# Optimization experiments

Hardware: AMD Instinct MI355X
Metric: run time of the kernel (lower is better)

Reference implementation:

```python
import jax, jax.numpy as jnp
import numpy as np

B, T, C = 2, 2048, 1024
NH = 16
HS = C // NH


def setup_inputs() -> dict:
    key = jax.random.key(0)
    k1, k2, k3 = jax.random.split(key, 3)
    scale = 1.0 / np.sqrt(C)
    return {
        "x": jax.random.normal(k1, (B, T, C), dtype=jnp.float32),
        "W_attn": jax.random.normal(k2, (C, 3 * C), dtype=jnp.float32) * scale,
        "b_attn": jnp.zeros((3 * C,), dtype=jnp.float32),
        "W_proj": jax.random.normal(k3, (C, C), dtype=jnp.float32) * scale,
        "b_proj": jnp.zeros((C,), dtype=jnp.float32),
    }


def reference(x, W_attn, b_attn, W_proj, b_proj) -> jnp.ndarray:
    Bx, Tx, Cx = x.shape
    qkv = x @ W_attn + b_attn                      # [B, T, 3C]
    q, k, v = jnp.split(qkv, 3, axis=-1)           # each [B, T, C]

    def heads(t):  # [B, T, C] -> [B, NH, T, HS]
        return t.reshape(Bx, Tx, NH, HS).transpose(0, 2, 1, 3)

    q, k, v = heads(q), heads(k), heads(v)
    att = jnp.einsum("bhqd,bhkd->bhqk", q, k) / jnp.sqrt(jnp.float32(HS))
    causal = jnp.tril(jnp.ones((Tx, Tx), dtype=bool))
    att = jnp.where(causal, att, -jnp.inf)
    att = jax.nn.softmax(att, axis=-1)
    y = jnp.einsum("bhqk,bhkd->bhqd", att, v)      # [B, NH, T, HS]
    y = y.transpose(0, 2, 1, 3).reshape(Bx, Tx, Cx)
    return y @ W_proj + b_proj
```

## Files before the change

### kernel.cpp

```cpp
#include <hip/hip_runtime.h>
#include <hip/hip_bf16.h>
#include <stdint.h>

#define DEV static __device__ __forceinline__

typedef __attribute__((ext_vector_type(8))) __bf16 bf16x8;
typedef __attribute__((ext_vector_type(4))) __bf16 bf16x4;
typedef __attribute__((ext_vector_type(4))) float f32x4;
typedef __attribute__((ext_vector_type(16))) float f32x16;

#define BB 2
#define TT 2048
#define CC 1024
#define NHH 16
#define HSS 64
#define BT 4096
#define N3 3072

DEV unsigned short f2bf(float f) {
  union { float f; uint32_t u; } v; v.f = f;
  uint32_t r = v.u + 0x7FFFu + ((v.u >> 16) & 1u);
  return (unsigned short)(r >> 16);
}

typedef const __attribute__((address_space(1))) unsigned int* gas_t;
typedef __attribute__((address_space(3))) unsigned int* las_t;

DEV void glds16(const void* g, void* l) {
  __builtin_amdgcn_global_load_lds((gas_t)g, (las_t)l, 16, 0, 0);
}

DEV f32x4 mfma16(bf16x8 a, bf16x8 b, f32x4 c) {
  return __builtin_amdgcn_mfma_f32_16x16x32_bf16(a, b, c, 0, 0, 0);
}
DEV f32x16 mfma32(bf16x8 a, bf16x8 b, f32x16 c) {
  return __builtin_amdgcn_mfma_f32_32x32x16_bf16(a, b, c, 0, 0, 0);
}

DEV bf16x8 ld8(const unsigned short* p) { return *(const bf16x8*)p; }

DEV f32x16 z16() {
  f32x16 v;
#pragma unroll
  for (int i = 0; i < 16; i++) v[i] = 0.f;
  return v;
}

__global__ void k_conv(const float* __restrict__ in, unsigned short* __restrict__ out, int n4) {
  int i = blockIdx.x * blockDim.x + threadIdx.x;
  int stride = gridDim.x * blockDim.x;
  for (; i < n4; i += stride) {
    float4 v = ((const float4*)in)[i];
    ushort4 o;
    o.x = f2bf(v.x); o.y = f2bf(v.y); o.z = f2bf(v.z); o.w = f2bf(v.w);
    ((ushort4*)out)[i] = o;
  }
}

__global__ void k_transp(const float* __restrict__ in, unsigned short* __restrict__ out,
                         int K, int N) {
  __shared__ float tile[32][33];
  int n0 = blockIdx.x * 32, k0 = blockIdx.y * 32;
  int tx = threadIdx.x, ty = threadIdx.y;
  for (int r = ty; r < 32; r += 8)
    tile[r][tx] = in[(size_t)(k0 + r) * N + n0 + tx];
  __syncthreads();
  for (int r = ty; r < 32; r += 8)
    out[(size_t)(n0 + r) * K + k0 + tx] = f2bf(tile[tx][r]);
}

template <int OUT_BF16>
__global__ __launch_bounds__(256) void k_gemm(const unsigned short* __restrict__ A,
                                              const unsigned short* __restrict__ Bt,
                                              const float* __restrict__ bias,
                                              void* __restrict__ Cout,
                                              int M, int N, int K) {
  __shared__ __align__(16) unsigned short As[128 * 32];
  __shared__ __align__(16) unsigned short Bs[128 * 32];
  const int t = threadIdx.x;
  const int wave = t >> 6, l = t & 63, lr = l & 15, lg = l >> 4;
  const int m0 = blockIdx.y * 128, n0 = blockIdx.x * 128;
  const int wm = wave >> 1, wn = wave & 1;

  f32x4 acc[4][4] = {};

  const unsigned short* gA = A + (size_t)(m0 + (t >> 2)) * K + (t & 3) * 8;
  const unsigned short* gB = Bt + (size_t)(n0 + (t >> 2)) * K + (t & 3) * 8;
  char* lA = (char*)As + wave * 1024;
  char* lB = (char*)Bs + wave * 1024;
  const size_t rstep = (size_t)64 * K;

  for (int k0 = 0; k0 < K; k0 += 32) {
    glds16(gA + k0, lA);
    glds16(gA + rstep + k0, lA + 4096);
    glds16(gB + k0, lB);
    glds16(gB + rstep + k0, lB + 4096);
    __syncthreads();
    bf16x8 av[4], bv[4];
#pragma unroll
    for (int i = 0; i < 4; i++) {
      av[i] = ld8(As + (wm * 64 + i * 16 + lr) * 32 + lg * 8);
      bv[i] = ld8(Bs + (wn * 64 + i * 16 + lr) * 32 + lg * 8);
    }
#pragma unroll
    for (int i = 0; i < 4; i++)
#pragma unroll
      for (int j = 0; j < 4; j++)
        acc[i][j] = mfma16(av[i], bv[j], acc[i][j]);
    __syncthreads();
  }

#pragma unroll
  for (int j2 = 0; j2 < 4; j2++) {
    int col = n0 + wn * 64 + j2 * 16 + lr;
    float bv_ = bias[col];
#pragma unroll
    for (int i = 0; i < 4; i++) {
      int row = m0 + wm * 64 + i * 16 + lg * 4;
#pragma unroll
      for (int r = 0; r < 4; r++) {
        float v = acc[i][j2][r] + bv_;
        if (OUT_BF16)
          ((unsigned short*)Cout)[(size_t)(row + r) * N + col] = f2bf(v);
        else
          ((float*)Cout)[(size_t)(row + r) * N + col] = v;
      }
    }
  }
}

__global__ void k_vt(const unsigned short* __restrict__ qkv, unsigned short* __restrict__ vt) {
  __shared__ unsigned short tile[64][65];
  int bh = blockIdx.y, t0 = blockIdx.x * 64;
  int b = bh >> 4, h = bh & 15;
  int tx = threadIdx.x, ty = threadIdx.y;
  const unsigned short* src = qkv + (size_t)(b * TT + t0) * N3 + 2 * CC + h * HSS;
  for (int r = ty; r < 64; r += 4)
    tile[r][tx] = src[(size_t)r * N3 + tx];
  __syncthreads();
  unsigned short* dst = vt + (size_t)bh * HSS * TT + t0;
  for (int r = ty; r < 64; r += 4)
    dst[(size_t)r * TT + tx] = tile[tx][r];
}

__global__ __launch_bounds__(512) void k_attn(const unsigned short* __restrict__ qkv,
                                              const unsigned short* __restrict__ vt,
                                              unsigned short* __restrict__ y) {
  __shared__ __align__(16) unsigned short Ks[3][128 * 64];
  __shared__ __align__(16) unsigned short Vs[3][128 * 64];
  __shared__ __align__(16) unsigned short Ps[8][32 * 64];
  __shared__ float Msh[4][64];
  __shared__ float Lsh[4][64];
  const int t = threadIdx.x;
  const int w = t >> 6, l = t & 63, lq = l & 31, hl = l >> 5;
  const int qsub = w & 3, par = w >> 2;
  const int id = blockIdx.x;
  const int bh = (id & 7) + 8 * ((id >> 3) & 3);
  const int p = id >> 5;
  const int b = bh >> 4, head = bh & 15;
  const int jA = 15 - p, jB = p;
  const int mA = jA + 1;
  const int NT = 17;
  const float cexp = 0.18033688011112042f;
  const float THR = 40.0f;

#define SWZ(r_) ((((r_) & 7) ^ (((r_) >> 3) & 3)) << 4)

  const int myswz = SWZ(lq);
  int offs[4];
#pragma unroll
  for (int s = 0; s < 4; s++) offs[s] = (32 * s + 16 * hl) ^ myswz;

  const int off0 = w * 1024 + l * 16;
  const int off1 = 8192 + w * 1024 + l * 16;
  const int rk0 = off0 >> 7, rk1 = off1 >> 7;
  const int ck0 = (off0 & 127) ^ SWZ(rk0), ck1 = (off1 & 127) ^ SWZ(rk1);
  const int rv0 = rk0 & 63, rv1 = rk1 & 63;
  const int cv0 = (off0 & 127) ^ SWZ(rv0), cv1 = (off1 & 127) ^ SWZ(rv1);
  const char* gK0 = (const char*)(qkv + (size_t)(b * TT + rk0) * N3 + CC + head * HSS) + ck0;
  const char* gK1 = (const char*)(qkv + (size_t)(b * TT + rk1) * N3 + CC + head * HSS) + ck1;
  const char* gV0 = (const char*)(vt + ((size_t)bh * HSS + rv0) * TT) + cv0;
  const char* gV1 = (const char*)(vt + ((size_t)bh * HSS + rv1) * TT + 64) + cv1;
  const int dK0 = w * 1024, dK1 = 8192 + w * 1024;

#define STAGE(slot_, kvt_)                                                \
  do {                                                                    \
    size_t kb = (size_t)(kvt_) * (128 * N3 * 2);                          \
    size_t vb = (size_t)(kvt_) * 256;                                     \
    glds16(gK0 + kb, (char*)Ks[slot_] + dK0);                             \
    glds16(gK1 + kb, (char*)Ks[slot_] + dK1);                             \
    glds16(gV0 + vb, (char*)Vs[slot_] + dK0);                             \
    glds16(gV1 + vb, (char*)Vs[slot_] + dK1);                             \
  } while (0)

#define WRITE_OUT()                                                       \
  do {                                                                    \
    float l_q = l_ln + __shfl_xor(l_ln, 32);                              \
    float inv = 1.0f / l_q;                                               \
    unsigned short* ybase = y + (size_t)(b * TT + q0w + lq) * CC + head * HSS; \
    _Pragma("unroll")                                                     \
    for (int g = 0; g < 4; g++) {                                         \
      ushort4 wv;                                                         \
      wv.x = f2bf(oa[4 * g + 0] * inv); wv.y = f2bf(oa[4 * g + 1] * inv); \
      wv.z = f2bf(oa[4 * g + 2] * inv); wv.w = f2bf(oa[4 * g + 3] * inv); \
      *(ushort4*)(ybase + 8 * g + 4 * hl) = wv;                           \
      ushort4 wv2;                                                        \
      wv2.x = f2bf(ob[4 * g + 0] * inv); wv2.y = f2bf(ob[4 * g + 1] * inv); \
      wv2.z = f2bf(ob[4 * g + 2] * inv); wv2.w = f2bf(ob[4 * g + 3] * inv); \
      *(ushort4*)(ybase + 32 + 8 * g + 4 * hl) = wv2;                     \
    }                                                                     \
  } while (0)

#define MERGE()                                                           \
  do {                                                                    \
    __builtin_amdgcn_s_barrier();                                         \
    if (par) {                                                            \
      float* poa = (float*)Ps[w];                                         \
      float* pob = (float*)Ps[w - 4];                                     \
      _Pragma("unroll")                                                   \
      for (int g = 0; g < 16; g++) { poa[g * 64 + l] = oa[g]; pob[g * 64 + l] = ob[g]; } \
      Msh[qsub][l] = m_s; Lsh[qsub][l] = l_ln;                            \
    }                                                                     \
    asm volatile("s_waitcnt lgkmcnt(0)" ::: "memory");                    \
    __builtin_amdgcn_s_barrier();                                         \
    __builtin_amdgcn_sched_barrier(0);                                    \
    if (!par) {                                                           \
      float m1 = Msh[qsub][l], l1 = Lsh[qsub][l];                         \
      float mstar = fmaxf(m_s, m1);                                       \
      float a0 = __builtin_amdgcn_exp2f((m_s - mstar) * cexp);            \
      float a1 = __builtin_amdgcn_exp2f((m1 - mstar) * cexp);             \
      const float* poa = (const float*)Ps[w + 4];                         \
      const float* pob = (const float*)Ps[w];                             \
      _Pragma("unroll")                                                   \
      for (int g = 0; g < 16; g++) {                                      \
        oa[g] = oa[g] * a0 + poa[g * 64 + l] * a1;                        \
        ob[g] = ob[g] * a0 + pob[g * 64 + l] * a1;                        \
      }                                                                   \
      l_ln = l_ln * a0 + l1 * a1;                                         \
      WRITE_OUT();                                                        \
    }                                                                     \
    __builtin_amdgcn_s_barrier();                                         \
  } while (0)

  int q0w = jA * 128 + qsub * 32;
  const unsigned short* qp = qkv + (size_t)(b * TT + q0w + lq) * N3 + head * HSS + hl * 8;
  bf16x8 qf0 = ld8(qp), qf1 = ld8(qp + 16), qf2 = ld8(qp + 32), qf3 = ld8(qp + 48);
  float m_s = -INFINITY, l_ln = 0.f;
  f32x16 oa = z16(), ob = z16();
  char* prow = (char*)Ps[w] + lq * 128;

  STAGE(0, 0);
  int cur = 0;

  for (int seq = 0; seq < NT; ++seq) {
    if (seq == mA) {
      MERGE();
      q0w = jB * 128 + qsub * 32;
      const unsigned short* qp2 = qkv + (size_t)(b * TT + q0w + lq) * N3 + head * HSS + hl * 8;
      qf0 = ld8(qp2); qf1 = ld8(qp2 + 16); qf2 = ld8(qp2 + 32); qf3 = ld8(qp2 + 48);
      m_s = -INFINITY; l_ln = 0.f;
      oa = z16(); ob = z16();
    }

    const int kvt = (seq < mA) ? seq : (seq - mA);
    if (seq + 1 < NT) {
      int s2 = seq + 1;
      int kvt2 = (s2 < mA) ? s2 : (s2 - mA);
      int nxt = (cur == 2) ? 0 : cur + 1;
      STAGE(nxt, kvt2);
      __builtin_amdgcn_sched_barrier(0);
      asm volatile("s_waitcnt vmcnt(4)" ::: "memory");
    } else {
      asm volatile("s_waitcnt vmcnt(0)" ::: "memory");
    }
    __builtin_amdgcn_s_barrier();
    __builtin_amdgcn_sched_barrier(0);

    const int mybuf = cur;
    cur = (cur == 2) ? 0 : cur + 1;

    const int kv0w = kvt * 128 + 64 * par;
    if (kv0w > q0w + 31) continue;

    const unsigned short* Kb = Ks[mybuf];
    const unsigned short* Vb = Vs[mybuf];

    const char* krA = (const char*)Kb + (64 * par + lq) * 128;
    const char* krB = krA + 32 * 128;
    f32x16 sa = z16(), sb = z16();
    __builtin_amdgcn_s_setprio(1);
    {
      bf16x8 ka, kb8;
      ka = ld8((const unsigned short*)(krA + offs[0]));
      kb8 = ld8((const unsigned short*)(krB + offs[0]));
      sa = mfma32(ka, qf0, sa); sb = mfma32(kb8, qf0, sb);
      ka = ld8((const unsigned short*)(krA + offs[1]));
      kb8 = ld8((const unsigned short*)(krB + offs[1]));
      sa = mfma32(ka, qf1, sa); sb = mfma32(kb8, qf1, sb);
      ka = ld8((const unsigned short*)(krA + offs[2]));
      kb8 = ld8((const unsigned short*)(krB + offs[2]));
      sa = mfma32(ka, qf2, sa); sb = mfma32(kb8, qf2, sb);
      ka = ld8((const unsigned short*)(krA + offs[3]));
      kb8 = ld8((const unsigned short*)(krB + offs[3]));
      sa = mfma32(ka, qf3, sa); sb = mfma32(kb8, qf3, sb);
    }
    __builtin_amdgcn_s_setprio(0);

    if (kv0w + 63 > q0w) {
      const int q = q0w + lq;
#pragma unroll
      for (int g = 0; g < 16; g++) {
        int kvl = kv0w + (g & 3) + 8 * (g >> 2) + 4 * hl;
        if (kvl > q) sa[g] = -INFINITY;
        if (kvl + 32 > q) sb[g] = -INFINITY;
      }
    }

    float tmax = -INFINITY;
#pragma unroll
    for (int g = 0; g < 16; g++) tmax = fmaxf(tmax, fmaxf(sa[g], sb[g]));
    tmax = fmaxf(tmax, __shfl_xor(tmax, 32));

    if (!__all(tmax <= m_s + THR)) {
      float m_new = fmaxf(m_s, tmax);
      float alpha = __builtin_amdgcn_exp2f((m_s - m_new) * cexp);
      l_ln *= alpha;
#pragma unroll
      for (int g = 0; g < 16; g++) { oa[g] *= alpha; ob[g] *= alpha; }
      m_s = m_new;
    }

    const float mc = m_s * cexp;
    float tsum = 0.f;
#pragma unroll
    for (int g = 0; g < 16; g++) {
      sa[g] = __builtin_amdgcn_exp2f(__builtin_fmaf(sa[g], cexp, -mc));
      sb[g] = __builtin_amdgcn_exp2f(__builtin_fmaf(sb[g], cexp, -mc));
      tsum += sa[g] + sb[g];
    }
    l_ln += tsum;

#pragma unroll
    for (int u2 = 0; u2 < 4; u2++) {
      bf16x4 w0, w1;
#pragma unroll
      for (int r = 0; r < 4; r++) { w0[r] = (__bf16)sa[4 * u2 + r]; w1[r] = (__bf16)sb[4 * u2 + r]; }
      *(bf16x4*)(prow + ((16 * u2 + 8 * hl) ^ myswz)) = w0;
      *(bf16x4*)(prow + ((64 + 16 * u2 + 8 * hl) ^ myswz)) = w1;
    }
    asm volatile("s_waitcnt lgkmcnt(0)" ::: "memory");
    __builtin_amdgcn_sched_barrier(0);
    bf16x8 pf0 = ld8((const unsigned short*)(prow + offs[0]));
    bf16x8 pf1 = ld8((const unsigned short*)(prow + offs[1]));
    bf16x8 pf2 = ld8((const unsigned short*)(prow + offs[2]));
    bf16x8 pf3 = ld8((const unsigned short*)(prow + offs[3]));

    const char* vrA = (const char*)Vb + par * 8192 + lq * 128;
    const char* vrB = vrA + 32 * 128;
    __builtin_amdgcn_s_setprio(1);
    {
      bf16x8 va, vb8;
      va = ld8((const unsigned short*)(vrA + offs[0]));
      vb8 = ld8((const unsigned short*)(vrB + offs[0]));
      oa = mfma32(va, pf0, oa); ob = mfma32(vb8, pf0, ob);
      va = ld8((const unsigned short*)(vrA + offs[1]));
      vb8 = ld8((const unsigned short*)(vrB + offs[1]));
      oa = mfma32(va, pf1, oa); ob = mfma32(vb8, pf1, ob);
      va = ld8((const unsigned short*)(vrA + offs[2]));
      vb8 = ld8((const unsigned short*)(vrB + offs[2]));
      oa = mfma32(va, pf2, oa); ob = mfma32(vb8, pf2, ob);
      va = ld8((const unsigned short*)(vrA + offs[3]));
      vb8 = ld8((const unsigned short*)(vrB + offs[3]));
      oa = mfma32(va, pf3, oa); ob = mfma32(vb8, pf3, ob);
    }
    __builtin_amdgcn_s_setprio(0);
  }

  MERGE();
#undef STAGE
#undef WRITE_OUT
#undef MERGE
#undef SWZ
}

extern "C" void kernel_launch(void* const* d_in, const int* in_sizes, int n_in,
                              void* d_out, int out_size, void* d_ws, size_t ws_size,
                              hipStream_t stream) {
  const float* x = (const float*)d_in[0];
  const float* W_attn = (const float*)d_in[1];
  const float* b_attn = (const float*)d_in[2];
  const float* W_proj = (const float*)d_in[3];
  const float* b_proj = (const float*)d_in[4];

  char* ws = (char*)d_ws;
  unsigned short* xb   = (unsigned short*)(ws);
  unsigned short* wabt = (unsigned short*)(ws + 8388608);
  unsigned short* wpbt = (unsigned short*)(ws + 14680064);
  unsigned short* qkvb = (unsigned short*)(ws + 16777216);
  unsigned short* vt   = (unsigned short*)(ws + 41943040);
  unsigned short* yb   = (unsigned short*)(ws + 50331648);

  k_conv<<<2048, 256, 0, stream>>>(x, xb, BT * CC / 4);
  k_transp<<<dim3(N3 / 32, CC / 32), dim3(32, 8), 0, stream>>>(W_attn, wabt, CC, N3);
  k_transp<<<dim3(CC / 32, CC / 32), dim3(32, 8), 0, stream>>>(W_proj, wpbt, CC, CC);
  k_gemm<1><<<dim3(N3 / 128, BT / 128), 256, 0, stream>>>(xb, wabt, b_attn, qkvb, BT, N3, CC);
  k_vt<<<dim3(TT / 64, BB * NHH), dim3(64, 4), 0, stream>>>(qkvb, vt);
  k_attn<<<dim3(256), 512, 0, stream>>>(qkvb, vt, yb);
  k_gemm<0><<<dim3(CC / 128, BT / 128), 256, 0, stream>>>(yb, wpbt, b_proj, d_out, BT, CC, CC);
}
```

Baseline: 125.0 us.

## Double-buffer GEMM LDS tiles and remap blocks across XCDs

The GEMM kernel now uses two LDS buffers. It issues the global-to-LDS loads for the next K slice before computing on the current one, so memory latency overlaps with MFMA work and each iteration needs one barrier instead of two. The grid is flattened to 1D and block IDs are remapped so each XCD gets a contiguous chunk of tiles, which is meant to improve L2 reuse. The cost is twice the LDS per block, which may lower occupancy, plus manual waitcnt and barrier handling.

```diff
diff --git a/kernel.cpp b/kernel.cpp
--- a/kernel.cpp
+++ b/kernel.cpp
@@ -74,41 +74,56 @@
                                               const unsigned short* __restrict__ Bt,
                                               const float* __restrict__ bias,
                                               void* __restrict__ Cout,
-                                              int M, int N, int K) {
-  __shared__ __align__(16) unsigned short As[128 * 32];
-  __shared__ __align__(16) unsigned short Bs[128 * 32];
+                                              int N, int K, int gx) {
+  __shared__ __align__(16) unsigned short As[2][128 * 32];
+  __shared__ __align__(16) unsigned short Bs[2][128 * 32];
   const int t = threadIdx.x;
   const int wave = t >> 6, l = t & 63, lr = l & 15, lg = l >> 4;
-  const int m0 = blockIdx.y * 128, n0 = blockIdx.x * 128;
+  const int cpx = gridDim.x >> 3;
+  const int sw = ((int)blockIdx.x & 7) * cpx + ((int)blockIdx.x >> 3);
+  const int m0 = (sw / gx) * 128, n0 = (sw % gx) * 128;
   const int wm = wave >> 1, wn = wave & 1;
 
   f32x4 acc[4][4] = {};
 
   const unsigned short* gA = A + (size_t)(m0 + (t >> 2)) * K + (t & 3) * 8;
   const unsigned short* gB = Bt + (size_t)(n0 + (t >> 2)) * K + (t & 3) * 8;
-  char* lA = (char*)As + wave * 1024;
-  char* lB = (char*)Bs + wave * 1024;
   const size_t rstep = (size_t)64 * K;
 
+#define GSTAGE(buf_, k_)                                                  \
+  do {                                                                    \
+    glds16(gA + (k_), (char*)As[buf_] + wave * 1024);                     \
+    glds16(gA + rstep + (k_), (char*)As[buf_] + 4096 + wave * 1024);      \
+    glds16(gB + (k_), (char*)Bs[buf_] + wave * 1024);                     \
+    glds16(gB + rstep + (k_), (char*)Bs[buf_] + 4096 + wave * 1024);      \
+  } while (0)
+
+  GSTAGE(0, 0);
+  asm volatile("s_waitcnt vmcnt(0)" ::: "memory");
+  __builtin_amdgcn_s_barrier();
+  __builtin_amdgcn_sched_barrier(0);
+
+  int cur = 0;
   for (int k0 = 0; k0 < K; k0 += 32) {
-    glds16(gA + k0, lA);
-    glds16(gA + rstep + k0, lA + 4096);
-    glds16(gB + k0, lB);
-    glds16(gB + rstep + k0, lB + 4096);
-    __syncthreads();
+    if (k0 + 32 < K) GSTAGE(cur ^ 1, k0 + 32);
+    __builtin_amdgcn_sched_barrier(0);
     bf16x8 av[4], bv[4];
 #pragma unroll
     for (int i = 0; i < 4; i++) {
-      av[i] = ld8(As + (wm * 64 + i * 16 + lr) * 32 + lg * 8);
-      bv[i] = ld8(Bs + (wn * 64 + i * 16 + lr) * 32 + lg * 8);
+      av[i] = ld8(As[cur] + (wm * 64 + i * 16 + lr) * 32 + lg * 8);
+      bv[i] = ld8(Bs[cur] + (wn * 64 + i * 16 + lr) * 32 + lg * 8);
     }
 #pragma unroll
     for (int i = 0; i < 4; i++)
 #pragma unroll
       for (int j = 0; j < 4; j++)
         acc[i][j] = mfma16(av[i], bv[j], acc[i][j]);
-    __syncthreads();
+    if (k0 + 32 < K) asm volatile("s_waitcnt vmcnt(0)" ::: "memory");
+    __builtin_amdgcn_s_barrier();
+    __builtin_amdgcn_sched_barrier(0);
+    cur ^= 1;
   }
+#undef GSTAGE
 
 #pragma unroll
   for (int j2 = 0; j2 < 4; j2++) {
@@ -403,8 +418,8 @@
   k_conv<<<2048, 256, 0, stream>>>(x, xb, BT * CC / 4);
   k_transp<<<dim3(N3 / 32, CC / 32), dim3(32, 8), 0, stream>>>(W_attn, wabt, CC, N3);
   k_transp<<<dim3(CC / 32, CC / 32), dim3(32, 8), 0, stream>>>(W_proj, wpbt, CC, CC);
-  k_gemm<1><<<dim3(N3 / 128, BT / 128), 256, 0, stream>>>(xb, wabt, b_attn, qkvb, BT, N3, CC);
+  k_gemm<1><<<dim3(768), 256, 0, stream>>>(xb, wabt, b_attn, qkvb, N3, CC, 24);
   k_vt<<<dim3(TT / 64, BB * NHH), dim3(64, 4), 0, stream>>>(qkvb, vt);
   k_attn<<<dim3(256), 512, 0, stream>>>(qkvb, vt, yb);
-  k_gemm<0><<<dim3(CC / 128, BT / 128), 256, 0, stream>>>(yb, wpbt, b_proj, d_out, BT, CC, CC);
-}
+  k_gemm<0><<<dim3(256), 256, 0, stream>>>(yb, wpbt, b_proj, d_out, CC, CC, 8);
+}
```

Result: faster. 116.1 us (-7.1%).
